# Kernel optimization log

Measured on AMD Instinct MI355X. Metric: run time of the kernel, lower is better.

The kernel has to match this reference:

```python
import jax, jax.numpy as jnp
import numpy as np

# ---- geometry / discretization constants (match init_kwargs) ----
IMG_H, IMG_W = 512, 512
N_VIEWS = 180
N_DET = 512
DET_SPACING = 2.0
VOXEL_SPACING = 1.0
SID = 600.0          # source-to-isocenter distance
IDD = 500.0          # isocenter-to-detector distance
N_SAMPLES = 512      # ray-marching samples per ray (Joseph-style)


def _bilinear(img, px, py):
    """Bilinear sample of 2D image at pixel coords (px=cols, py=rows); 0 outside."""
    H, W = img.shape
    ix0 = jnp.floor(px)
    iy0 = jnp.floor(py)
    fx = px - ix0
    fy = py - iy0
    ix0 = ix0.astype(jnp.int32)
    iy0 = iy0.astype(jnp.int32)
    ix1 = ix0 + 1
    iy1 = iy0 + 1
    flat = img.reshape(-1)

    def gather(iy, ix):
        valid = (ix >= 0) & (ix < W) & (iy >= 0) & (iy < H)
        idx = jnp.clip(iy, 0, H - 1) * W + jnp.clip(ix, 0, W - 1)
        return jnp.where(valid, jnp.take(flat, idx), 0.0)

    return (gather(iy0, ix0) * (1.0 - fx) * (1.0 - fy)
            + gather(iy0, ix1) * fx * (1.0 - fy)
            + gather(iy1, ix0) * (1.0 - fx) * fy
            + gather(iy1, ix1) * fx * fy)


def fan_project(img, src_pos, det_center, det_u_vec):
    """Fan-beam forward projection: line integrals src -> each detector bin.
    img: [H,W]; src_pos/det_center/det_u_vec: [V,2]. Returns sinogram [V,n_det]."""
    H, W = img.shape
    # detector bin offsets along the detector tangent, centered
    u = (jnp.arange(N_DET, dtype=img.dtype) - (N_DET - 1) / 2.0) * DET_SPACING  # [D]
    det_pts = det_center[:, None, :] + u[None, :, None] * det_u_vec[:, None, :]  # [V,D,2]
    src = src_pos[:, None, :]                                                    # [V,1,2]
    d = det_pts - src                                                            # [V,D,2]
    seg_len = jnp.sqrt(d[..., 0] ** 2 + d[..., 1] ** 2)                          # [V,D]
    # midpoint samples t in (0,1) along each ray
    t = (jnp.arange(N_SAMPLES, dtype=img.dtype) + 0.5) / N_SAMPLES               # [S]
    pts_x = src[..., 0][:, :, None] + t[None, None, :] * d[..., 0][:, :, None]   # [V,D,S]
    pts_y = src[..., 1][:, :, None] + t[None, None, :] * d[..., 1][:, :, None]   # [V,D,S]
    # world -> pixel coords (image centered at origin)
    px = pts_x / VOXEL_SPACING + (W - 1) / 2.0
    py = pts_y / VOXEL_SPACING + (H - 1) / 2.0
    vals = _bilinear(img, px, py)                                                # [V,D,S]
    return vals.sum(axis=-1) * (seg_len / N_SAMPLES)                             # [V,D]


def setup_inputs() -> dict:
    key = jax.random.key(0)
    k1, k2 = jax.random.split(key)
    x = jax.random.normal(k1, (IMG_H, IMG_W), dtype=jnp.float32)
    reco = jax.random.normal(k2, (IMG_H, IMG_W), dtype=jnp.float32) * 0.01
    ang = np.linspace(0.0, 2.0 * np.pi, N_VIEWS, endpoint=False).astype(np.float32)
    cos_a, sin_a = np.cos(ang), np.sin(ang)
    src_pos = jnp.asarray(np.stack([SID * cos_a, SID * sin_a], axis=-1))
    det_center = jnp.asarray(np.stack([-IDD * cos_a, -IDD * sin_a], axis=-1))
    det_u_vec = jnp.asarray(np.stack([-sin_a, cos_a], axis=-1))
    return {"x": x, "reco": reco, "src_pos": src_pos,
            "det_center": det_center, "det_u_vec": det_u_vec}


def reference(x, reco, src_pos, det_center, det_u_vec):
    updated = x + reco
    sino = fan_project(updated, src_pos, det_center, det_u_vec)
    return sino, jax.nn.relu(updated)
```

## Files before the change

kernel.cpp:

```cpp
#include <hip/hip_runtime.h>
#include <hip/hip_bf16.h>
#include <hip/hip_fp16.h>

#define IMG_H 512
#define IMG_W 512
#define N_VIEWS 180
#define N_DET 512
#define N_SAMPLES 512

#define N_RAYS (N_VIEWS * N_DET)
#define IMG_N (IMG_H * IMG_W)

#define QPAD 8
#define QDIM (IMG_W + 1 + 2 * QPAD)
#define R_N (QDIM * QDIM)
#define R_BYTES ((size_t)R_N * 4)
#define R_BYTES_AL ((R_BYTES + 255) & ~(size_t)255)
#define RAYINFO_BYTES ((size_t)N_RAYS * 32)

#define K_CHUNKS 4
#define PACK_BLOCKS ((R_N + 255) / 256)
#define SETUP_BLOCKS (N_RAYS / 256)

__global__ __launch_bounds__(256) void prep_kernel(
        const float* __restrict__ x, const float* __restrict__ r,
        unsigned* __restrict__ R, float* __restrict__ relu_out,
        const float* __restrict__ src_pos,
        const float* __restrict__ det_center,
        const float* __restrict__ det_u,
        float4* __restrict__ RA, float4* __restrict__ RB,
        float* __restrict__ sino) {
    const int b = blockIdx.x;
    if (b < PACK_BLOCKS) {
        int i = b * 256 + threadIdx.x;
        if (i >= R_N) return;
        int row = i / QDIM;
        int col = i - row * QDIM;
        int yy = row - QPAD;
        int xx = col - QPAD;
        float v0 = 0.f, v1 = 0.f;
        if ((unsigned)xx < (unsigned)IMG_W) {
            if ((unsigned)yy < (unsigned)IMG_H) {
                int idx = yy * IMG_W + xx;
                v0 = x[idx] + r[idx];
            }
            if ((unsigned)(yy + 1) < (unsigned)IMG_H) {
                int idx = (yy + 1) * IMG_W + xx;
                v1 = x[idx] + r[idx];
            }
        }
        __half2 h = __floats2half2_rn(v0, v1);
        R[i] = *reinterpret_cast<unsigned*>(&h);
        if ((unsigned)xx < (unsigned)IMG_W && (unsigned)yy < (unsigned)IMG_H)
            relu_out[yy * IMG_W + xx] = fmaxf(v0, 0.f);
        return;
    }

    const int rid = (b - PACK_BLOCKS) * 256 + threadIdx.x;
    const int v   = rid >> 9;
    const int det = rid & 511;

    const float sx = src_pos[2 * v];
    const float sy = src_pos[2 * v + 1];
    const float u  = ((float)det - 255.5f) * 2.0f;
    const float ex = det_center[2 * v]     + u * det_u[2 * v];
    const float ey = det_center[2 * v + 1] + u * det_u[2 * v + 1];

    const float dx = ex - sx;
    const float dy = ey - sy;
    const float segscl = sqrtf(dx * dx + dy * dy) * (1.0f / (float)N_SAMPLES);

    const float lo = -256.5f, hi = 256.5f;
    float t0 = 0.f, t1 = 1.f;
    if (fabsf(dx) > 1e-12f) {
        float ta = (lo - sx) / dx, tb = (hi - sx) / dx;
        t0 = fmaxf(t0, fminf(ta, tb));
        t1 = fminf(t1, fmaxf(ta, tb));
    } else if (sx <= lo || sx >= hi) {
        t1 = -1.f;
    }
    if (fabsf(dy) > 1e-12f) {
        float ta = (lo - sy) / dy, tb = (hi - sy) / dy;
        t0 = fmaxf(t0, fminf(ta, tb));
        t1 = fminf(t1, fmaxf(ta, tb));
    } else if (sy <= lo || sy >= hi) {
        t1 = -1.f;
    }
    int s0 = 0, len = 0;
    if (t1 >= t0) {
        s0 = max(0, (int)floorf(t0 * (float)N_SAMPLES - 0.5f) - 1);
        int s1 = min(N_SAMPLES - 1, (int)ceilf(t1 * (float)N_SAMPLES - 0.5f) + 1);
        len = s1 - s0 + 1;
        if (len < 0) len = 0;
    }
    RA[rid] = make_float4(dx, dy, sx + 255.5f + (float)QPAD,
                                  sy + 255.5f + (float)QPAD);
    RB[rid] = make_float4(segscl, (float)s0, (float)len, 0.f);
    sino[rid] = 0.f;
}

__device__ __forceinline__ float sample_h(const unsigned* __restrict__ R,
                                          float t, float dx, float dy,
                                          float bx, float by, float acc) {
    const float px = fmaf(t, dx, bx);
    const float py = fmaf(t, dy, by);
    const float ixf = truncf(px);
    const float iyf = truncf(py);
    const float fx = px - ixf;
    const float fy = py - iyf;
    const float linf = fmaf(iyf, (float)QDIM, ixf);
    const int lin = (int)linf;

    uint2 qw;
    __builtin_memcpy(&qw, R + lin, 8);
    const float2 fa = __half22float2(*reinterpret_cast<const __half2*>(&qw.x));
    const float2 fb = __half22float2(*reinterpret_cast<const __half2*>(&qw.y));

    const float gx = 1.f - fx;
    const float h0 = fmaf(fx, fb.x, gx * fa.x);
    const float h1 = fmaf(fx, fb.y, gx * fa.y);
    acc = fmaf(1.f - fy, h0, acc);
    acc = fmaf(fy, h1, acc);
    return acc;
}

__global__ __launch_bounds__(256) void fanproj_tile_kernel(
        const unsigned* __restrict__ R,
        const float4* __restrict__ RA, const float4* __restrict__ RB,
        float* __restrict__ sino) {
    const int tix  = threadIdx.x;
    const int lane = tix & 63;
    const int dsub = lane & 15;
    const int soff = lane >> 4;
    const int rid  = blockIdx.x * 64 + ((tix >> 6) << 4) + dsub;
    const int chunk = blockIdx.y;

    const float4 a = RA[rid];
    const float4 b = RB[rid];
    const float dx = a.x, dy = a.y, bx = a.z, by = a.w;
    const int s0  = (int)b.y;
    const int len = (int)b.z;
    const int c0 = s0 + ((len * chunk) >> 2);
    const int c1 = s0 + ((len * (chunk + 1)) >> 2) - 1;

    int s = c0 + soff;
    float t = ((float)s + 0.5f) * (1.0f / (float)N_SAMPLES);
    float acc0 = 0.f, acc1 = 0.f, acc2 = 0.f, acc3 = 0.f;
    for (; s + 12 <= c1; s += 16) {
        acc0 = sample_h(R, t,               dx, dy, bx, by, acc0);
        acc1 = sample_h(R, t + 0.0078125f,  dx, dy, bx, by, acc1);
        acc2 = sample_h(R, t + 0.015625f,   dx, dy, bx, by, acc2);
        acc3 = sample_h(R, t + 0.0234375f,  dx, dy, bx, by, acc3);
        t += 0.03125f;
    }
    for (; s <= c1; s += 4) {
        acc0 = sample_h(R, t, dx, dy, bx, by, acc0);
        t += 0.0078125f;
    }

    float acc = (acc0 + acc1) + (acc2 + acc3);
    acc += __shfl_xor(acc, 16);
    acc += __shfl_xor(acc, 32);
    if (soff == 0) {
        const float res = acc * b.x;
        if (res != 0.f) atomicAdd(&sino[rid], res);
    }
}

__global__ __launch_bounds__(256) void add_kernel(const float4* __restrict__ x,
                                                  const float4* __restrict__ r,
                                                  float4* __restrict__ upd) {
    int i = blockIdx.x * blockDim.x + threadIdx.x;
    float4 a = x[i];
    float4 b = r[i];
    upd[i] = make_float4(a.x + b.x, a.y + b.y, a.z + b.z, a.w + b.w);
}
__global__ __launch_bounds__(256) void relu_kernel(const float4* __restrict__ upd,
                                                   float4* __restrict__ out) {
    int i = blockIdx.x * blockDim.x + threadIdx.x;
    float4 c = upd[i];
    out[i] = make_float4(fmaxf(c.x, 0.f), fmaxf(c.y, 0.f),
                         fmaxf(c.z, 0.f), fmaxf(c.w, 0.f));
}

__device__ __forceinline__ float sample_plain(const float* __restrict__ img,
                                              int s, float dx, float dy,
                                              float bx, float by, float acc) {
    const float t  = fmaf((float)s, 1.f / (float)N_SAMPLES,
                          0.5f / (float)N_SAMPLES);
    const float px = fmaf(t, dx, bx);
    const float py = fmaf(t, dy, by);
    const float ix0f = floorf(px);
    const float iy0f = floorf(py);
    const float fx = px - ix0f;
    const float fy = py - iy0f;
    const int ix0 = (int)ix0f;
    const int iy0 = (int)iy0f;
    const float gx = ((unsigned)ix0       < (unsigned)IMG_W) ? (1.f - fx) : 0.f;
    const float hx = ((unsigned)(ix0 + 1) < (unsigned)IMG_W) ? fx         : 0.f;
    const float gy = ((unsigned)iy0       < (unsigned)IMG_H) ? (1.f - fy) : 0.f;
    const float hy = ((unsigned)(iy0 + 1) < (unsigned)IMG_H) ? fy         : 0.f;
    const unsigned cx0 = (unsigned)min(max(ix0, 0), IMG_W - 1);
    const unsigned cx1 = (unsigned)min(max(ix0 + 1, 0), IMG_W - 1);
    const unsigned r0  = (unsigned)min(max(iy0, 0), IMG_H - 1) << 9;
    const unsigned r1  = (unsigned)min(max(iy0 + 1, 0), IMG_H - 1) << 9;
    const float v00 = img[r0 + cx0];
    const float v01 = img[r0 + cx1];
    const float v10 = img[r1 + cx0];
    const float v11 = img[r1 + cx1];
    acc = fmaf(v00, gx * gy, acc);
    acc = fmaf(v01, hx * gy, acc);
    acc = fmaf(v10, gx * hy, acc);
    acc = fmaf(v11, hx * hy, acc);
    return acc;
}

__global__ __launch_bounds__(256) void fanproj_plain_kernel(
        const float* __restrict__ img,
        const float* __restrict__ src_pos,
        const float* __restrict__ det_center,
        const float* __restrict__ det_u,
        float* __restrict__ sino) {
    const int wid  = (blockIdx.x * blockDim.x + threadIdx.x) >> 6;
    const int lane = threadIdx.x & 63;
    if (wid >= N_RAYS) return;
    const int v   = wid >> 9;
    const int det = wid & 511;
    const float sx = src_pos[2 * v];
    const float sy = src_pos[2 * v + 1];
    const float u  = ((float)det - 255.5f) * 2.0f;
    const float ex = det_center[2 * v]     + u * det_u[2 * v];
    const float ey = det_center[2 * v + 1] + u * det_u[2 * v + 1];
    const float dx = ex - sx;
    const float dy = ey - sy;
    const float seg = sqrtf(dx * dx + dy * dy);
    const float bx = sx + 255.5f;
    const float by = sy + 255.5f;
    const float lo = -256.5f, hi = 256.5f;
    float t0 = 0.f, t1 = 1.f;
    if (fabsf(dx) > 1e-12f) {
        float ta = (lo - sx) / dx, tb = (hi - sx) / dx;
        t0 = fmaxf(t0, fminf(ta, tb));
        t1 = fminf(t1, fmaxf(ta, tb));
    } else if (sx <= lo || sx >= hi) {
        t1 = -1.f;
    }
    if (fabsf(dy) > 1e-12f) {
        float ta = (lo - sy) / dy, tb = (hi - sy) / dy;
        t0 = fmaxf(t0, fminf(ta, tb));
        t1 = fminf(t1, fmaxf(ta, tb));
    } else if (sy <= lo || sy >= hi) {
        t1 = -1.f;
    }
    int s0 = 0, s1 = -1;
    if (t1 >= t0) {
        s0 = max(0, (int)floorf(t0 * (float)N_SAMPLES - 0.5f) - 1);
        s1 = min(N_SAMPLES - 1, (int)ceilf(t1 * (float)N_SAMPLES - 0.5f) + 1);
    }
    float acc0 = 0.f, acc1 = 0.f;
    int s = s0 + lane;
    for (; s + 64 <= s1; s += 128) {
        acc0 = sample_plain(img, s,      dx, dy, bx, by, acc0);
        acc1 = sample_plain(img, s + 64, dx, dy, bx, by, acc1);
    }
    if (s <= s1) acc0 = sample_plain(img, s, dx, dy, bx, by, acc0);
    float acc = acc0 + acc1;
    #pragma unroll
    for (int off = 32; off >= 1; off >>= 1) acc += __shfl_xor(acc, off);
    if (lane == 0) sino[wid] = acc * seg * (1.0f / (float)N_SAMPLES);
}

extern "C" void kernel_launch(void* const* d_in, const int* in_sizes, int n_in,
                              void* d_out, int out_size, void* d_ws, size_t ws_size,
                              hipStream_t stream) {
    const float* x          = (const float*)d_in[0];
    const float* reco       = (const float*)d_in[1];
    const float* src_pos    = (const float*)d_in[2];
    const float* det_center = (const float*)d_in[3];
    const float* det_u      = (const float*)d_in[4];

    float* out  = (float*)d_out;
    float* sino = out;
    float* relu = out + N_RAYS;

    const int n4 = IMG_N / 4;

    if (ws_size >= R_BYTES_AL + RAYINFO_BYTES) {
        unsigned* R  = (unsigned*)d_ws;
        float4*   RA = (float4*)((char*)d_ws + R_BYTES_AL);
        float4*   RB = RA + N_RAYS;
        prep_kernel<<<PACK_BLOCKS + SETUP_BLOCKS, 256, 0, stream>>>(
            x, reco, R, relu, src_pos, det_center, det_u, RA, RB, sino);
        fanproj_tile_kernel<<<dim3(N_RAYS / 64, K_CHUNKS), 256, 0, stream>>>(
            R, RA, RB, sino);
    } else {
        float* upd = relu;
        add_kernel<<<n4 / 256, 256, 0, stream>>>(
            (const float4*)x, (const float4*)reco, (float4*)upd);
        fanproj_plain_kernel<<<N_RAYS / 4, 256, 0, stream>>>(
            upd, src_pos, det_center, det_u, sino);
        relu_kernel<<<n4 / 256, 256, 0, stream>>>(
            (const float4*)upd, (float4*)relu);
    }
}
```

Measured before the change: 36.93 us.

## Add transposed half2 image copy and pick layout per view orientation

Builds a second packed fp16 image in column-major (transposed) order next to the row-major one. Each ray picks the copy whose fast axis best matches its direction, swapping its x/y coordinates to suit, so consecutive samples along a ray hit nearby memory and cache locality improves for near-vertical views. The cost is an extra pack pass in the prep kernel, double the workspace, and a per-ray pointer select in the projection kernel.

Result: slower. 38.00 us (+2.9%).

```diff
diff --git a/kernel.cpp b/kernel.cpp
--- a/kernel.cpp
+++ b/kernel.cpp
@@ -24,7 +24,8 @@
 
 __global__ __launch_bounds__(256) void prep_kernel(
         const float* __restrict__ x, const float* __restrict__ r,
-        unsigned* __restrict__ R, float* __restrict__ relu_out,
+        unsigned* __restrict__ Rrm, unsigned* __restrict__ Tcm,
+        float* __restrict__ relu_out,
         const float* __restrict__ src_pos,
         const float* __restrict__ det_center,
         const float* __restrict__ det_u,
@@ -50,21 +51,46 @@
             }
         }
         __half2 h = __floats2half2_rn(v0, v1);
-        R[i] = *reinterpret_cast<unsigned*>(&h);
+        Rrm[i] = *reinterpret_cast<unsigned*>(&h);
         if ((unsigned)xx < (unsigned)IMG_W && (unsigned)yy < (unsigned)IMG_H)
             relu_out[yy * IMG_W + xx] = fmaxf(v0, 0.f);
         return;
     }
-
-    const int rid = (b - PACK_BLOCKS) * 256 + threadIdx.x;
+    if (b < 2 * PACK_BLOCKS) {
+        int j = (b - PACK_BLOCKS) * 256 + threadIdx.x;
+        if (j >= R_N) return;
+        int row = j / QDIM;
+        int col = j - row * QDIM;
+        int rp = row - QPAD;
+        int cp = col - QPAD;
+        float v0 = 0.f, v1 = 0.f;
+        if ((unsigned)cp < (unsigned)IMG_H) {
+            int base = cp * IMG_W;
+            if ((unsigned)rp < (unsigned)IMG_W)       v0 = x[base + rp] + r[base + rp];
+            if ((unsigned)(rp + 1) < (unsigned)IMG_W) v1 = x[base + rp + 1] + r[base + rp + 1];
+        }
+        __half2 h = __floats2half2_rn(v0, v1);
+        Tcm[j] = *reinterpret_cast<unsigned*>(&h);
+        return;
+    }
+
+    const int rid = (b - 2 * PACK_BLOCKS) * 256 + threadIdx.x;
     const int v   = rid >> 9;
     const int det = rid & 511;
 
-    const float sx = src_pos[2 * v];
-    const float sy = src_pos[2 * v + 1];
+    float sx = src_pos[2 * v];
+    float sy = src_pos[2 * v + 1];
+    const float ux = det_u[2 * v];
+    const float uy = det_u[2 * v + 1];
     const float u  = ((float)det - 255.5f) * 2.0f;
-    const float ex = det_center[2 * v]     + u * det_u[2 * v];
-    const float ey = det_center[2 * v + 1] + u * det_u[2 * v + 1];
+    float ex = det_center[2 * v]     + u * ux;
+    float ey = det_center[2 * v + 1] + u * uy;
+
+    const bool useT = fabsf(uy) > fabsf(ux);
+    if (useT) {
+        float tmp = sx; sx = sy; sy = tmp;
+        tmp = ex; ex = ey; ey = tmp;
+    }
 
     const float dx = ex - sx;
     const float dy = ey - sy;
@@ -95,7 +121,7 @@
     }
     RA[rid] = make_float4(dx, dy, sx + 255.5f + (float)QPAD,
                                   sy + 255.5f + (float)QPAD);
-    RB[rid] = make_float4(segscl, (float)s0, (float)len, 0.f);
+    RB[rid] = make_float4(segscl, (float)s0, (float)len, useT ? 1.f : 0.f);
     sino[rid] = 0.f;
 }
 
@@ -125,7 +151,7 @@
 }
 
 __global__ __launch_bounds__(256) void fanproj_tile_kernel(
-        const unsigned* __restrict__ R,
+        const unsigned* __restrict__ Rrm, const unsigned* __restrict__ Tcm,
         const float4* __restrict__ RA, const float4* __restrict__ RB,
         float* __restrict__ sino) {
     const int tix  = threadIdx.x;
@@ -140,6 +166,7 @@
     const float dx = a.x, dy = a.y, bx = a.z, by = a.w;
     const int s0  = (int)b.y;
     const int len = (int)b.z;
+    const unsigned* __restrict__ R = (b.w != 0.f) ? Tcm : Rrm;
     const int c0 = s0 + ((len * chunk) >> 2);
     const int c1 = s0 + ((len * (chunk + 1)) >> 2) - 1;
 
@@ -285,14 +312,15 @@
 
     const int n4 = IMG_N / 4;
 
-    if (ws_size >= R_BYTES_AL + RAYINFO_BYTES) {
-        unsigned* R  = (unsigned*)d_ws;
-        float4*   RA = (float4*)((char*)d_ws + R_BYTES_AL);
-        float4*   RB = RA + N_RAYS;
-        prep_kernel<<<PACK_BLOCKS + SETUP_BLOCKS, 256, 0, stream>>>(
-            x, reco, R, relu, src_pos, det_center, det_u, RA, RB, sino);
+    if (ws_size >= 2 * R_BYTES_AL + RAYINFO_BYTES) {
+        unsigned* Rrm = (unsigned*)d_ws;
+        unsigned* Tcm = (unsigned*)((char*)d_ws + R_BYTES_AL);
+        float4*   RA  = (float4*)((char*)d_ws + 2 * R_BYTES_AL);
+        float4*   RB  = RA + N_RAYS;
+        prep_kernel<<<2 * PACK_BLOCKS + SETUP_BLOCKS, 256, 0, stream>>>(
+            x, reco, Rrm, Tcm, relu, src_pos, det_center, det_u, RA, RB, sino);
         fanproj_tile_kernel<<<dim3(N_RAYS / 64, K_CHUNKS), 256, 0, stream>>>(
-            R, RA, RB, sino);
+            Rrm, Tcm, RA, RB, sino);
     } else {
         float* upd = relu;
         add_kernel<<<n4 / 256, 256, 0, stream>>>(
```
